# Performance work log

Measured on AMD Instinct MI355X. Metric: run time of the kernel, lower is better.

## Reference

```python
import jax, jax.numpy as jnp
import numpy as np

HEADS = 8
D_MODEL = 512
D_K = D_MODEL // HEADS


def setup_inputs() -> dict:
    key = jax.random.key(0)
    ks = jax.random.split(key, 12)
    B, S = 2, 4096
    scale = 1.0 / np.sqrt(D_MODEL)
    inp = {
        "q": jax.random.normal(ks[0], (B, S, D_MODEL), jnp.float32),
        "k": jax.random.normal(ks[1], (B, S, D_MODEL), jnp.float32),
        "v": jax.random.normal(ks[2], (B, S, D_MODEL), jnp.float32),
        "mask": jax.random.randint(ks[3], (B, 1, 1, S), 0, 2, jnp.int32),
        "wq": jax.random.normal(ks[4], (D_MODEL, D_MODEL), jnp.float32) * scale,
        "bq": jnp.zeros((D_MODEL,), jnp.float32),
        "wk": jax.random.normal(ks[5], (D_MODEL, D_MODEL), jnp.float32) * scale,
        "bk": jnp.zeros((D_MODEL,), jnp.float32),
        "wv": jax.random.normal(ks[6], (D_MODEL, D_MODEL), jnp.float32) * scale,
        "bv": jnp.zeros((D_MODEL,), jnp.float32),
        "wo": jax.random.normal(ks[7], (D_MODEL, D_MODEL), jnp.float32) * scale,
        "bo": jnp.zeros((D_MODEL,), jnp.float32),
    }
    return inp


def reference(q, k, v, mask, wq, bq, wk, bk, wv, bv, wo, bo):
    B, S, _ = q.shape
    # torch nn.Linear: y = x @ W.T + b
    qh = (q @ wq.T + bq).reshape(B, S, HEADS, D_K).transpose(0, 2, 1, 3)  # b h s d
    kh = (k @ wk.T + bk).reshape(B, S, HEADS, D_K).transpose(0, 2, 1, 3)
    vh = (v @ wv.T + bv).reshape(B, S, HEADS, D_K).transpose(0, 2, 1, 3)
    scores = jnp.einsum("bhqd,bhkd->bhqk", qh, kh) / jnp.sqrt(jnp.float32(D_K))
    scores = jnp.where(mask == 0, jnp.float32(-1e9), scores)
    attn = jax.nn.softmax(scores, axis=-1)  # dropout is identity in eval mode
    out = jnp.einsum("bhqk,bhkd->bhqd", attn, vh)
    out = out.transpose(0, 2, 1, 3).reshape(B, S, D_MODEL)
    return out @ wo.T + bo
```

## Files before the change

### kernel.cpp

```cpp
#include <hip/hip_runtime.h>
#include <hip/hip_bf16.h>

#define S 4096
#define DM 512
#define HH 8
#define DK 64
#define MT 8192

typedef __attribute__((ext_vector_type(8)))  short bf16x8;
typedef __attribute__((ext_vector_type(4)))  float f32x4;
typedef __attribute__((ext_vector_type(16))) float f32x16;
typedef __attribute__((ext_vector_type(4)))  unsigned int u32x4;

#define CQ 0.18033688011112042f

__device__ __forceinline__ short f2bs(float x) {
    __hip_bfloat16 h = __float2bfloat16(x);
    return *reinterpret_cast<short*>(&h);
}

__device__ __forceinline__ bf16x8 pack8(const float4& a, const float4& b) {
    bf16x8 r;
    r[0] = f2bs(a.x); r[1] = f2bs(a.y); r[2] = f2bs(a.z); r[3] = f2bs(a.w);
    r[4] = f2bs(b.x); r[5] = f2bs(b.y); r[6] = f2bs(b.z); r[7] = f2bs(b.w);
    return r;
}

__device__ __forceinline__ unsigned cvtpk(float lo, float hi) {
    unsigned r;
    asm("v_cvt_pk_bf16_f32 %0, %1, %2" : "=v"(r) : "v"(lo), "v"(hi));
    return r;
}

__device__ __forceinline__ bf16x8 mk_pb(unsigned a, unsigned b, unsigned c, unsigned d) {
    u32x4 t; t[0] = a; t[1] = b; t[2] = c; t[3] = d;
    return __builtin_bit_cast(bf16x8, t);
}

__device__ __forceinline__ void gld_lds16(const void* gp, void* lp) {
    __builtin_amdgcn_global_load_lds(
        (const __attribute__((address_space(1))) void*)gp,
        (__attribute__((address_space(3))) void*)lp, 16, 0, 0);
}

__global__ __launch_bounds__(256, 4)
void qkv_gemm(const float* __restrict__ Xq, const float* __restrict__ Xk,
              const float* __restrict__ Xv,
              const float* __restrict__ Wq, const float* __restrict__ Wk,
              const float* __restrict__ Wv,
              const float* __restrict__ Bq, const float* __restrict__ Bk,
              const float* __restrict__ Bv,
              const int* __restrict__ mask, float* __restrict__ maskf,
              unsigned short* __restrict__ Yq, unsigned short* __restrict__ Yk,
              unsigned short* __restrict__ Yv)
{
    __shared__ char As[128 * 128];
    __shared__ char Bs[64 * 128];
    const int bid  = blockIdx.x;
    const int t = threadIdx.x;
    if (bid < 32) {
        int i = bid * 256 + t;
        maskf[i] = mask[i] ? 0.f : -3e38f;
    }
    const int work = (bid & 7) * 192 + (bid >> 3);
    const int gp   = work >> 3;
    const int mat  = gp >> 6;
    const int m0   = (gp & 63) * 128;
    const int n0   = (work & 7) * 64;
    const float* X    = mat == 0 ? Xq : (mat == 1 ? Xk : Xv);
    const float* W    = mat == 0 ? Wq : (mat == 1 ? Wk : Wv);
    const float* bias = mat == 0 ? Bq : (mat == 1 ? Bk : Bv);

    const int l = t & 63, w = t >> 6;
    const int wr = w >> 1, wc = w & 1;
    const int lr = l & 15, lg = l >> 4;
    const int srow = t >> 3, schk = t & 7;
    const int sswz = (schk ^ (srow & 7)) * 16;

    float4 fA[4][2]; float4 fB[2][2];
    auto loadA = [&](int k0) {
        #pragma unroll
        for (int i = 0; i < 4; ++i) {
            const float* p = X + (size_t)(m0 + srow + 32 * i) * DM + k0 + schk * 8;
            fA[i][0] = *(const float4*)p;
            fA[i][1] = *(const float4*)(p + 4);
        }
    };
    auto loadB = [&](int k0) {
        #pragma unroll
        for (int i = 0; i < 2; ++i) {
            const float* p = W + (size_t)(n0 + srow + 32 * i) * DM + k0 + schk * 8;
            fB[i][0] = *(const float4*)p;
            fB[i][1] = *(const float4*)(p + 4);
        }
    };

    loadA(0); loadB(0);

    f32x4 acc[4][2];
    #pragma unroll
    for (int fm = 0; fm < 4; ++fm)
        #pragma unroll
        for (int fn = 0; fn < 2; ++fn) acc[fm][fn] = f32x4{0.f, 0.f, 0.f, 0.f};

    #pragma unroll
    for (int kt = 0; kt < 8; ++kt) {
        bf16x8 wA[4], wB[2];
        #pragma unroll
        for (int i = 0; i < 4; ++i) wA[i] = pack8(fA[i][0], fA[i][1]);
        #pragma unroll
        for (int i = 0; i < 2; ++i) wB[i] = pack8(fB[i][0], fB[i][1]);

        if (kt < 7) { loadA((kt + 1) * 64); loadB((kt + 1) * 64); }

        __syncthreads();
        #pragma unroll
        for (int i = 0; i < 4; ++i)
            *(bf16x8*)(As + (srow + 32 * i) * 128 + sswz) = wA[i];
        #pragma unroll
        for (int i = 0; i < 2; ++i)
            *(bf16x8*)(Bs + (srow + 32 * i) * 128 + sswz) = wB[i];
        __syncthreads();

        #pragma unroll
        for (int kc = 0; kc < 2; ++kc) {
            bf16x8 af[4], bfr[2];
            #pragma unroll
            for (int fm = 0; fm < 4; ++fm) {
                int row = wr * 64 + fm * 16 + lr;
                af[fm] = *(const bf16x8*)(As + row * 128 + (((kc * 4 + lg) ^ (row & 7)) * 16));
            }
            #pragma unroll
            for (int fn = 0; fn < 2; ++fn) {
                int row = wc * 32 + fn * 16 + lr;
                bfr[fn] = *(const bf16x8*)(Bs + row * 128 + (((kc * 4 + lg) ^ (row & 7)) * 16));
            }
            #pragma unroll
            for (int fm = 0; fm < 4; ++fm)
                #pragma unroll
                for (int fn = 0; fn < 2; ++fn)
                    acc[fm][fn] = __builtin_amdgcn_mfma_f32_16x16x32_bf16(af[fm], bfr[fn], acc[fm][fn], 0, 0, 0);
        }
    }

    #pragma unroll
    for (int fm = 0; fm < 4; ++fm) {
        #pragma unroll
        for (int fn = 0; fn < 2; ++fn) {
            int n = n0 + wc * 32 + fn * 16 + lr;
            float bn = bias[n];
            int mbase = m0 + wr * 64 + fm * 16 + lg * 4;
            int h = n >> 6, d = n & 63;
            int bb = mbase >> 12, s0 = mbase & (S - 1);
            if (mat == 0) {
                #pragma unroll
                for (int r = 0; r < 4; ++r)
                    Yq[(((size_t)(bb * HH + h)) * S + s0 + r) * DK + d] =
                        (unsigned short)f2bs((acc[fm][fn][r] + bn) * CQ);
            } else if (mat == 1) {
                int c   = (d >> 4) & 3;
                int hi2 = (d >> 3) & 1;
                int ii  = d & 7;
                size_t blkb = ((((size_t)(bb * HH + h)) * 128 + (s0 >> 5)) * 4 + c) * 512;
                int lanebase = (s0 & 31) + 32 * hi2;
                #pragma unroll
                for (int r = 0; r < 4; ++r)
                    Yk[blkb + (size_t)(lanebase + r) * 8 + ii] =
                        (unsigned short)f2bs(acc[fm][fn][r] + bn);
            } else {
                int dt2  = (d >> 5) & 1;
                int hi_s = (s0 >> 3) & 1;
                int lane = (d & 31) + 32 * hi_s;
                size_t base = ((((size_t)(bb * HH + h)) * 256 + (s0 >> 4)) * 2 + dt2) * 512
                            + (size_t)lane * 8 + (s0 & 7);
                ushort4 u;
                u.x = (unsigned short)f2bs(acc[fm][fn][0] + bn);
                u.y = (unsigned short)f2bs(acc[fm][fn][1] + bn);
                u.z = (unsigned short)f2bs(acc[fm][fn][2] + bn);
                u.w = (unsigned short)f2bs(acc[fm][fn][3] + bn);
                *(ushort4*)(Yv + base) = u;
            }
        }
    }
}

__global__ __launch_bounds__(256, 2)
void out_gemm(const short* __restrict__ Xb, const float* __restrict__ W,
              const float* __restrict__ bias, float* __restrict__ Y)
{
    __shared__ char As[128 * 128];
    __shared__ char Bs[64 * 128];
    const int bid  = blockIdx.x;
    const int work = (bid & 7) * 64 + (bid >> 3);
    const int n0 = (work & 7) * 64;
    const int m0 = (work >> 3) * 128;

    const int t = threadIdx.x, l = t & 63, w = t >> 6;
    const int wr = w >> 1, wc = w & 1;
    const int lr = l & 15, lg = l >> 4;
    const int srow = t >> 3, schk = t & 7;
    const int sswz = (schk ^ (srow & 7)) * 16;

    float4 fB[2][2]; bf16x8 rA[4];
    auto loadA = [&](int k0) {
        #pragma unroll
        for (int i = 0; i < 4; ++i)
            rA[i] = *(const bf16x8*)(Xb + (size_t)(m0 + srow + 32 * i) * DM + k0 + schk * 8);
    };
    auto loadB = [&](int k0) {
        #pragma unroll
        for (int i = 0; i < 2; ++i) {
            const float* p = W + (size_t)(n0 + srow + 32 * i) * DM + k0 + schk * 8;
            fB[i][0] = *(const float4*)p;
            fB[i][1] = *(const float4*)(p + 4);
        }
    };

    loadA(0); loadB(0);

    f32x4 acc[4][2];
    #pragma unroll
    for (int fm = 0; fm < 4; ++fm)
        #pragma unroll
        for (int fn = 0; fn < 2; ++fn) acc[fm][fn] = f32x4{0.f, 0.f, 0.f, 0.f};

    #pragma unroll
    for (int kt = 0; kt < 8; ++kt) {
        bf16x8 wA[4], wB[2];
        #pragma unroll
        for (int i = 0; i < 4; ++i) wA[i] = rA[i];
        #pragma unroll
        for (int i = 0; i < 2; ++i) wB[i] = pack8(fB[i][0], fB[i][1]);

        if (kt < 7) { loadA((kt + 1) * 64); loadB((kt + 1) * 64); }

        __syncthreads();
        #pragma unroll
        for (int i = 0; i < 4; ++i)
            *(bf16x8*)(As + (srow + 32 * i) * 128 + sswz) = wA[i];
        #pragma unroll
        for (int i = 0; i < 2; ++i)
            *(bf16x8*)(Bs + (srow + 32 * i) * 128 + sswz) = wB[i];
        __syncthreads();

        #pragma unroll
        for (int kc = 0; kc < 2; ++kc) {
            bf16x8 af[4], bfr[2];
            #pragma unroll
            for (int fm = 0; fm < 4; ++fm) {
                int row = wr * 64 + fm * 16 + lr;
                af[fm] = *(const bf16x8*)(As + row * 128 + (((kc * 4 + lg) ^ (row & 7)) * 16));
            }
            #pragma unroll
            for (int fn = 0; fn < 2; ++fn) {
                int row = wc * 32 + fn * 16 + lr;
                bfr[fn] = *(const bf16x8*)(Bs + row * 128 + (((kc * 4 + lg) ^ (row & 7)) * 16));
            }
            #pragma unroll
            for (int fm = 0; fm < 4; ++fm)
                #pragma unroll
                for (int fn = 0; fn < 2; ++fn)
                    acc[fm][fn] = __builtin_amdgcn_mfma_f32_16x16x32_bf16(af[fm], bfr[fn], acc[fm][fn], 0, 0, 0);
        }
    }

    #pragma unroll
    for (int fm = 0; fm < 4; ++fm) {
        #pragma unroll
        for (int fn = 0; fn < 2; ++fn) {
            int n = n0 + wc * 32 + fn * 16 + lr;
            float bn = bias[n];
            int mbase = m0 + wr * 64 + fm * 16 + lg * 4;
            #pragma unroll
            for (int r = 0; r < 4; ++r)
                Y[(size_t)(mbase + r) * DM + n] = acc[fm][fn][r] + bn;
        }
    }
}

__global__ __launch_bounds__(512, 4)
void flash_mfma(const short* __restrict__ qh,
                const short* __restrict__ kfb,
                const short* __restrict__ vfb,
                const float* __restrict__ maskf,
                unsigned short* __restrict__ att)
{
    const int bid  = blockIdx.x;
    const int work = (bid & 7) * 64 + (bid >> 3);
    const int bh = work >> 5, b = bh >> 3, h = bh & 7;
    const int q0 = (work & 31) * 128;
    const int t = threadIdx.x, w = t >> 6, l = t & 63;
    const int l31 = l & 31, hi = l >> 5;
    const int kw = w & 1, qw = w >> 1;

    __shared__ char sBuf[34048];
    char* B0 = sBuf;
    char* B1 = sBuf + 16384;

    const short* qg = qh + ((size_t)bh * S + q0 + qw * 32 + l31) * DK;
    bf16x8 qf[4];
    #pragma unroll
    for (int c = 0; c < 4; ++c)
        qf[c] = *(const bf16x8*)(qg + c * 16 + hi * 8);

    f32x16 oc[2];
    #pragma unroll
    for (int dt = 0; dt < 2; ++dt)
        #pragma unroll
        for (int r = 0; r < 16; ++r) oc[dt][r] = 0.f;
    float ls = 0.f;

    const char* kg0 = (const char*)(kfb + (size_t)bh * 262144) + (size_t)l * 16;
    const char* vg0 = (const char*)(vfb + (size_t)bh * 262144) + (size_t)l * 16;
    const float* mbase_g = maskf + b * S + kw * 32 + hi * 4;

    auto stage = [&](char* dst, int step) {
        const char* kg = kg0 + (size_t)step * 8192;
        const char* vg = vg0 + (size_t)step * 8192;
        #pragma unroll
        for (int i = 0; i < 2; ++i) {
            int chunk = w * 2 + i;
            const char* g = (chunk < 8) ? (kg + chunk * 1024) : (vg + (chunk - 8) * 1024);
            gld_lds16(g, dst + chunk * 1024);
        }
    };

    auto compute = [&](const char* kv, int step) {
        const float* mp = mbase_g + step * 64;
        f32x16 sc;
        float* scp = (float*)&sc;
        *(f32x4*)(scp + 0)  = *(const f32x4*)(mp);
        *(f32x4*)(scp + 4)  = *(const f32x4*)(mp + 8);
        *(f32x4*)(scp + 8)  = *(const f32x4*)(mp + 16);
        *(f32x4*)(scp + 12) = *(const f32x4*)(mp + 24);

        const char* kbase = kv + kw * 4096 + l * 16;
        bf16x8 kf0 = *(const bf16x8*)(kbase);
        bf16x8 kf1 = *(const bf16x8*)(kbase + 1024);
        bf16x8 kf2 = *(const bf16x8*)(kbase + 2048);
        bf16x8 kf3 = *(const bf16x8*)(kbase + 3072);
        __builtin_amdgcn_s_setprio(1);
        sc = __builtin_amdgcn_mfma_f32_32x32x16_bf16(kf0, qf[0], sc, 0, 0, 0);
        sc = __builtin_amdgcn_mfma_f32_32x32x16_bf16(kf1, qf[1], sc, 0, 0, 0);
        sc = __builtin_amdgcn_mfma_f32_32x32x16_bf16(kf2, qf[2], sc, 0, 0, 0);
        sc = __builtin_amdgcn_mfma_f32_32x32x16_bf16(kf3, qf[3], sc, 0, 0, 0);
        __builtin_amdgcn_s_setprio(0);

        const char* vbase = kv + 8192 + kw * 4096 + l * 16;
        bf16x8 vf00 = *(const bf16x8*)(vbase);
        bf16x8 vf01 = *(const bf16x8*)(vbase + 1024);
        bf16x8 vf10 = *(const bf16x8*)(vbase + 2048);
        bf16x8 vf11 = *(const bf16x8*)(vbase + 3072);

        float p[16];
        #pragma unroll
        for (int r = 0; r < 16; ++r) p[r] = exp2f(sc[r]);
        float a0 = 0.f;
        #pragma unroll
        for (int r = 0; r < 16; r += 4)
            a0 += (p[r] + p[r + 1]) + (p[r + 2] + p[r + 3]);
        ls += a0;

        unsigned A0 = cvtpk(p[0],  p[1]),  B0r = cvtpk(p[2],  p[3]);
        unsigned A1 = cvtpk(p[4],  p[5]),  B1r = cvtpk(p[6],  p[7]);
        unsigned A2 = cvtpk(p[8],  p[9]),  B2r = cvtpk(p[10], p[11]);
        unsigned A3 = cvtpk(p[12], p[13]), B3r = cvtpk(p[14], p[15]);
        asm("v_permlane32_swap_b32 %0, %1" : "+v"(A0), "+v"(A1));
        asm("v_permlane32_swap_b32 %0, %1" : "+v"(B0r), "+v"(B1r));
        asm("v_permlane32_swap_b32 %0, %1" : "+v"(A2), "+v"(A3));
        asm("v_permlane32_swap_b32 %0, %1" : "+v"(B2r), "+v"(B3r));
        bf16x8 pb0 = mk_pb(A0, B0r, A1, B1r);
        bf16x8 pb1 = mk_pb(A2, B2r, A3, B3r);

        __builtin_amdgcn_s_setprio(1);
        oc[0] = __builtin_amdgcn_mfma_f32_32x32x16_bf16(vf00, pb0, oc[0], 0, 0, 0);
        oc[1] = __builtin_amdgcn_mfma_f32_32x32x16_bf16(vf01, pb0, oc[1], 0, 0, 0);
        oc[0] = __builtin_amdgcn_mfma_f32_32x32x16_bf16(vf10, pb1, oc[0], 0, 0, 0);
        oc[1] = __builtin_amdgcn_mfma_f32_32x32x16_bf16(vf11, pb1, oc[1], 0, 0, 0);
        __builtin_amdgcn_s_setprio(0);
    };

    stage(B0, 0);
    __syncthreads();

    const int NT = S / 64;
    for (int it = 0; it < NT / 2; ++it) {
        const int s0 = it * 2;
        stage(B1, s0 + 1);
        compute(B0, s0);
        __syncthreads();
        if (s0 + 2 < NT) stage(B0, s0 + 2);
        compute(B1, s0 + 1);
        __syncthreads();
    }

    float* scr = (float*)sBuf;
    float* pp  = scr + (size_t)(qw * 64 + l) * 33;
    if (kw == 1) {
        #pragma unroll
        for (int r = 0; r < 16; ++r) { pp[r] = oc[0][r]; pp[16 + r] = oc[1][r]; }
        pp[32] = ls;
    }
    __syncthreads();
    if (kw == 0) {
        #pragma unroll
        for (int r = 0; r < 16; ++r) { oc[0][r] += pp[r]; oc[1][r] += pp[16 + r]; }
        ls += pp[32];
        ls += __shfl_xor(ls, 32);
        const float linv = 1.0f / ls;
        unsigned short* ap = att + ((size_t)(b * S + q0 + qw * 32 + l31)) * DM + h * DK;
        #pragma unroll
        for (int dt = 0; dt < 2; ++dt)
            #pragma unroll
            for (int g = 0; g < 4; ++g) {
                uint2 u;
                u.x = cvtpk(oc[dt][g * 4 + 0] * linv, oc[dt][g * 4 + 1] * linv);
                u.y = cvtpk(oc[dt][g * 4 + 2] * linv, oc[dt][g * 4 + 3] * linv);
                *(uint2*)(ap + dt * 32 + g * 8 + hi * 4) = u;
            }
    }
}

extern "C" void kernel_launch(void* const* d_in, const int* in_sizes, int n_in,
                              void* d_out, int out_size, void* d_ws, size_t ws_size,
                              hipStream_t stream) {
    const float* q    = (const float*)d_in[0];
    const float* k    = (const float*)d_in[1];
    const float* v    = (const float*)d_in[2];
    const int*   mask = (const int*)  d_in[3];
    const float* wq   = (const float*)d_in[4];
    const float* bq   = (const float*)d_in[5];
    const float* wk   = (const float*)d_in[6];
    const float* bk   = (const float*)d_in[7];
    const float* wv   = (const float*)d_in[8];
    const float* bv   = (const float*)d_in[9];
    const float* wo   = (const float*)d_in[10];
    const float* bo   = (const float*)d_in[11];
    float* out = (float*)d_out;

    char* wsb = (char*)d_ws;
    unsigned short* qh    = (unsigned short*)(wsb);
    unsigned short* kfb   = (unsigned short*)(wsb + (size_t)8  * 1024 * 1024);
    unsigned short* vfb   = (unsigned short*)(wsb + (size_t)16 * 1024 * 1024);
    unsigned short* att   = (unsigned short*)(wsb + (size_t)24 * 1024 * 1024);
    float*          maskf = (float*)         (wsb + (size_t)32 * 1024 * 1024);

    dim3 blk(256);
    qkv_gemm<<<dim3(1536), blk, 0, stream>>>(q, k, v, wq, wk, wv, bq, bk, bv,
                                     mask, maskf, qh, kfb, vfb);

    flash_mfma<<<dim3(512), dim3(512), 0, stream>>>((const short*)qh, (const short*)kfb,
                                     (const short*)vfb, maskf, att);

    out_gemm<<<dim3(512), blk, 0, stream>>>((const short*)att, wo, bo, out);
}
```

Before: 163.6 us.

## Software-pipeline QK and softmax-PV across tiles; halve flash block to 256 threads

The flash attention kernel now runs 256-thread blocks covering 64 queries each, with twice as many blocks, and each warp stages four chunks per tile. The loop is restructured so the QK^T MFMAs for the next KV tile are issued before the softmax and PV MFMAs of the current tile, keeping two score accumulators and two V fragment sets live. This is meant to overlap exp/convert work with matrix ops and improve scheduling across the GPU. In exchange it raises register pressure, drops the occupancy hint in launch bounds, and doubles K/V reads from global memory per query.

```diff
diff --git a/kernel.cpp b/kernel.cpp
--- a/kernel.cpp
+++ b/kernel.cpp
@@ -278,7 +278,7 @@
     }
 }
 
-__global__ __launch_bounds__(512, 4)
+__global__ __launch_bounds__(256)
 void flash_mfma(const short* __restrict__ qh,
                 const short* __restrict__ kfb,
                 const short* __restrict__ vfb,
@@ -286,14 +286,14 @@
                 unsigned short* __restrict__ att)
 {
     const int bid  = blockIdx.x;
-    const int work = (bid & 7) * 64 + (bid >> 3);
-    const int bh = work >> 5, b = bh >> 3, h = bh & 7;
-    const int q0 = (work & 31) * 128;
+    const int work = (bid & 7) * 128 + (bid >> 3);
+    const int bh = work >> 6, b = bh >> 3, h = bh & 7;
+    const int q0 = (work & 63) * 64;
     const int t = threadIdx.x, w = t >> 6, l = t & 63;
     const int l31 = l & 31, hi = l >> 5;
     const int kw = w & 1, qw = w >> 1;
 
-    __shared__ char sBuf[34048];
+    __shared__ char sBuf[33792];
     char* B0 = sBuf;
     char* B1 = sBuf + 16384;
 
@@ -318,14 +318,27 @@
         const char* kg = kg0 + (size_t)step * 8192;
         const char* vg = vg0 + (size_t)step * 8192;
         #pragma unroll
-        for (int i = 0; i < 2; ++i) {
-            int chunk = w * 2 + i;
+        for (int i = 0; i < 4; ++i) {
+            int chunk = w * 4 + i;
             const char* g = (chunk < 8) ? (kg + chunk * 1024) : (vg + (chunk - 8) * 1024);
             gld_lds16(g, dst + chunk * 1024);
         }
     };
 
-    auto compute = [&](const char* kv, int step) {
+    auto loadfrags = [&](const char* kv, bf16x8* kf, bf16x8* vf) {
+        const char* kbase = kv + kw * 4096 + l * 16;
+        kf[0] = *(const bf16x8*)(kbase);
+        kf[1] = *(const bf16x8*)(kbase + 1024);
+        kf[2] = *(const bf16x8*)(kbase + 2048);
+        kf[3] = *(const bf16x8*)(kbase + 3072);
+        const char* vbase = kv + 8192 + kw * 4096 + l * 16;
+        vf[0] = *(const bf16x8*)(vbase);
+        vf[1] = *(const bf16x8*)(vbase + 1024);
+        vf[2] = *(const bf16x8*)(vbase + 2048);
+        vf[3] = *(const bf16x8*)(vbase + 3072);
+    };
+
+    auto qk = [&](const bf16x8* kf, int step) -> f32x16 {
         const float* mp = mbase_g + step * 64;
         f32x16 sc;
         float* scp = (float*)&sc;
@@ -333,25 +346,16 @@
         *(f32x4*)(scp + 4)  = *(const f32x4*)(mp + 8);
         *(f32x4*)(scp + 8)  = *(const f32x4*)(mp + 16);
         *(f32x4*)(scp + 12) = *(const f32x4*)(mp + 24);
-
-        const char* kbase = kv + kw * 4096 + l * 16;
-        bf16x8 kf0 = *(const bf16x8*)(kbase);
-        bf16x8 kf1 = *(const bf16x8*)(kbase + 1024);
-        bf16x8 kf2 = *(const bf16x8*)(kbase + 2048);
-        bf16x8 kf3 = *(const bf16x8*)(kbase + 3072);
         __builtin_amdgcn_s_setprio(1);
-        sc = __builtin_amdgcn_mfma_f32_32x32x16_bf16(kf0, qf[0], sc, 0, 0, 0);
-        sc = __builtin_amdgcn_mfma_f32_32x32x16_bf16(kf1, qf[1], sc, 0, 0, 0);
-        sc = __builtin_amdgcn_mfma_f32_32x32x16_bf16(kf2, qf[2], sc, 0, 0, 0);
-        sc = __builtin_amdgcn_mfma_f32_32x32x16_bf16(kf3, qf[3], sc, 0, 0, 0);
+        sc = __builtin_amdgcn_mfma_f32_32x32x16_bf16(kf[0], qf[0], sc, 0, 0, 0);
+        sc = __builtin_amdgcn_mfma_f32_32x32x16_bf16(kf[1], qf[1], sc, 0, 0, 0);
+        sc = __builtin_amdgcn_mfma_f32_32x32x16_bf16(kf[2], qf[2], sc, 0, 0, 0);
+        sc = __builtin_amdgcn_mfma_f32_32x32x16_bf16(kf[3], qf[3], sc, 0, 0, 0);
         __builtin_amdgcn_s_setprio(0);
-
-        const char* vbase = kv + 8192 + kw * 4096 + l * 16;
-        bf16x8 vf00 = *(const bf16x8*)(vbase);
-        bf16x8 vf01 = *(const bf16x8*)(vbase + 1024);
-        bf16x8 vf10 = *(const bf16x8*)(vbase + 2048);
-        bf16x8 vf11 = *(const bf16x8*)(vbase + 3072);
-
+        return sc;
+    };
+
+    auto sm_pv = [&](const f32x16& sc, const bf16x8* vf) {
         float p[16];
         #pragma unroll
         for (int r = 0; r < 16; ++r) p[r] = exp2f(sc[r]);
@@ -373,27 +377,49 @@
         bf16x8 pb1 = mk_pb(A2, B2r, A3, B3r);
 
         __builtin_amdgcn_s_setprio(1);
-        oc[0] = __builtin_amdgcn_mfma_f32_32x32x16_bf16(vf00, pb0, oc[0], 0, 0, 0);
-        oc[1] = __builtin_amdgcn_mfma_f32_32x32x16_bf16(vf01, pb0, oc[1], 0, 0, 0);
-        oc[0] = __builtin_amdgcn_mfma_f32_32x32x16_bf16(vf10, pb1, oc[0], 0, 0, 0);
-        oc[1] = __builtin_amdgcn_mfma_f32_32x32x16_bf16(vf11, pb1, oc[1], 0, 0, 0);
+        oc[0] = __builtin_amdgcn_mfma_f32_32x32x16_bf16(vf[0], pb0, oc[0], 0, 0, 0);
+        oc[1] = __builtin_amdgcn_mfma_f32_32x32x16_bf16(vf[1], pb0, oc[1], 0, 0, 0);
+        oc[0] = __builtin_amdgcn_mfma_f32_32x32x16_bf16(vf[2], pb1, oc[0], 0, 0, 0);
+        oc[1] = __builtin_amdgcn_mfma_f32_32x32x16_bf16(vf[3], pb1, oc[1], 0, 0, 0);
         __builtin_amdgcn_s_setprio(0);
     };
 
+    bf16x8 vfA[4], vfB[4];
+    f32x16 scA;
     stage(B0, 0);
     __syncthreads();
+    {
+        bf16x8 kf[4];
+        loadfrags(B0, kf, vfA);
+        scA = qk(kf, 0);
+    }
+    stage(B1, 1);
 
     const int NT = S / 64;
-    for (int it = 0; it < NT / 2; ++it) {
-        const int s0 = it * 2;
-        stage(B1, s0 + 1);
-        compute(B0, s0);
-        __syncthreads();
-        if (s0 + 2 < NT) stage(B0, s0 + 2);
-        compute(B1, s0 + 1);
-        __syncthreads();
-    }
-
+    for (int it2 = 0; it2 < NT / 2; ++it2) {
+        const int it = it2 * 2;
+
+        __syncthreads();
+        f32x16 scB;
+        {
+            bf16x8 kf[4];
+            loadfrags(B1, kf, vfB);
+            scB = qk(kf, it + 1);
+        }
+        if (it + 2 < NT) stage(B0, it + 2);
+        sm_pv(scA, vfA);
+
+        __syncthreads();
+        if (it + 2 < NT) {
+            bf16x8 kf[4];
+            loadfrags(B0, kf, vfA);
+            scA = qk(kf, it + 2);
+        }
+        if (it + 3 < NT) stage(B1, it + 3);
+        sm_pv(scB, vfB);
+    }
+
+    __syncthreads();
     float* scr = (float*)sBuf;
     float* pp  = scr + (size_t)(qw * 64 + l) * 33;
     if (kw == 1) {
@@ -449,7 +475,7 @@
     qkv_gemm<<<dim3(1536), blk, 0, stream>>>(q, k, v, wq, wk, wv, bq, bk, bv,
                                      mask, maskf, qh, kfb, vfb);
 
-    flash_mfma<<<dim3(512), dim3(512), 0, stream>>>((const short*)qh, (const short*)kfb,
+    flash_mfma<<<dim3(1024), blk, 0, stream>>>((const short*)qh, (const short*)kfb,
                                      (const short*)vfb, maskf, att);
 
     out_gemm<<<dim3(512), blk, 0, stream>>>((const short*)att, wo, bo, out);
```

After: 181.9 us. 11.1% more time.

## Drop KV-split across waves in flash kernel, each wave handles full 64-key tile

Applied to the files above, without the earlier changes.

The flash-attention kernel drops from 512 threads to 256 per block, so each wave now processes all 64 keys of a tile instead of splitting them between two waves. This removes the cross-wave LDS reduction and the extra barrier in the epilogue, and doubles the MFMA work per wave per tile. In exchange it halves the waves per block, lowering latency hiding and raising register pressure from the two score accumulators.

```diff
diff --git a/kernel.cpp b/kernel.cpp
--- a/kernel.cpp
+++ b/kernel.cpp
@@ -278,7 +278,7 @@
     }
 }
 
-__global__ __launch_bounds__(512, 4)
+__global__ __launch_bounds__(256, 4)
 void flash_mfma(const short* __restrict__ qh,
                 const short* __restrict__ kfb,
                 const short* __restrict__ vfb,
@@ -291,9 +291,9 @@
     const int q0 = (work & 31) * 128;
     const int t = threadIdx.x, w = t >> 6, l = t & 63;
     const int l31 = l & 31, hi = l >> 5;
-    const int kw = w & 1, qw = w >> 1;
-
-    __shared__ char sBuf[34048];
+    const int qw = w;
+
+    __shared__ char sBuf[32768];
     char* B0 = sBuf;
     char* B1 = sBuf + 16384;
 
@@ -312,14 +312,14 @@
 
     const char* kg0 = (const char*)(kfb + (size_t)bh * 262144) + (size_t)l * 16;
     const char* vg0 = (const char*)(vfb + (size_t)bh * 262144) + (size_t)l * 16;
-    const float* mbase_g = maskf + b * S + kw * 32 + hi * 4;
+    const float* mbase_g = maskf + b * S + hi * 4;
 
     auto stage = [&](char* dst, int step) {
         const char* kg = kg0 + (size_t)step * 8192;
         const char* vg = vg0 + (size_t)step * 8192;
         #pragma unroll
-        for (int i = 0; i < 2; ++i) {
-            int chunk = w * 2 + i;
+        for (int i = 0; i < 4; ++i) {
+            int chunk = w * 4 + i;
             const char* g = (chunk < 8) ? (kg + chunk * 1024) : (vg + (chunk - 8) * 1024);
             gld_lds16(g, dst + chunk * 1024);
         }
@@ -327,56 +327,101 @@
 
     auto compute = [&](const char* kv, int step) {
         const float* mp = mbase_g + step * 64;
-        f32x16 sc;
-        float* scp = (float*)&sc;
-        *(f32x4*)(scp + 0)  = *(const f32x4*)(mp);
-        *(f32x4*)(scp + 4)  = *(const f32x4*)(mp + 8);
-        *(f32x4*)(scp + 8)  = *(const f32x4*)(mp + 16);
-        *(f32x4*)(scp + 12) = *(const f32x4*)(mp + 24);
-
-        const char* kbase = kv + kw * 4096 + l * 16;
+        f32x16 sc0, sc1;
+        {
+            float* s0p = (float*)&sc0;
+            float* s1p = (float*)&sc1;
+            *(f32x4*)(s0p + 0)  = *(const f32x4*)(mp);
+            *(f32x4*)(s0p + 4)  = *(const f32x4*)(mp + 8);
+            *(f32x4*)(s0p + 8)  = *(const f32x4*)(mp + 16);
+            *(f32x4*)(s0p + 12) = *(const f32x4*)(mp + 24);
+            *(f32x4*)(s1p + 0)  = *(const f32x4*)(mp + 32);
+            *(f32x4*)(s1p + 4)  = *(const f32x4*)(mp + 40);
+            *(f32x4*)(s1p + 8)  = *(const f32x4*)(mp + 48);
+            *(f32x4*)(s1p + 12) = *(const f32x4*)(mp + 56);
+        }
+
+        const char* kbase = kv + l * 16;
         bf16x8 kf0 = *(const bf16x8*)(kbase);
+        bf16x8 kf4 = *(const bf16x8*)(kbase + 4096);
         bf16x8 kf1 = *(const bf16x8*)(kbase + 1024);
+        bf16x8 kf5 = *(const bf16x8*)(kbase + 5120);
         bf16x8 kf2 = *(const bf16x8*)(kbase + 2048);
+        bf16x8 kf6 = *(const bf16x8*)(kbase + 6144);
         bf16x8 kf3 = *(const bf16x8*)(kbase + 3072);
+        bf16x8 kf7 = *(const bf16x8*)(kbase + 7168);
         __builtin_amdgcn_s_setprio(1);
-        sc = __builtin_amdgcn_mfma_f32_32x32x16_bf16(kf0, qf[0], sc, 0, 0, 0);
-        sc = __builtin_amdgcn_mfma_f32_32x32x16_bf16(kf1, qf[1], sc, 0, 0, 0);
-        sc = __builtin_amdgcn_mfma_f32_32x32x16_bf16(kf2, qf[2], sc, 0, 0, 0);
-        sc = __builtin_amdgcn_mfma_f32_32x32x16_bf16(kf3, qf[3], sc, 0, 0, 0);
+        sc0 = __builtin_amdgcn_mfma_f32_32x32x16_bf16(kf0, qf[0], sc0, 0, 0, 0);
+        sc1 = __builtin_amdgcn_mfma_f32_32x32x16_bf16(kf4, qf[0], sc1, 0, 0, 0);
+        sc0 = __builtin_amdgcn_mfma_f32_32x32x16_bf16(kf1, qf[1], sc0, 0, 0, 0);
+        sc1 = __builtin_amdgcn_mfma_f32_32x32x16_bf16(kf5, qf[1], sc1, 0, 0, 0);
+        sc0 = __builtin_amdgcn_mfma_f32_32x32x16_bf16(kf2, qf[2], sc0, 0, 0, 0);
+        sc1 = __builtin_amdgcn_mfma_f32_32x32x16_bf16(kf6, qf[2], sc1, 0, 0, 0);
+        sc0 = __builtin_amdgcn_mfma_f32_32x32x16_bf16(kf3, qf[3], sc0, 0, 0, 0);
+        sc1 = __builtin_amdgcn_mfma_f32_32x32x16_bf16(kf7, qf[3], sc1, 0, 0, 0);
         __builtin_amdgcn_s_setprio(0);
 
-        const char* vbase = kv + 8192 + kw * 4096 + l * 16;
+        bf16x8 pbA0, pbA1, pbB0, pbB1;
+        {
+            float p[16];
+            #pragma unroll
+            for (int r = 0; r < 16; ++r) p[r] = exp2f(sc0[r]);
+            float a0 = 0.f;
+            #pragma unroll
+            for (int r = 0; r < 16; r += 4)
+                a0 += (p[r] + p[r + 1]) + (p[r + 2] + p[r + 3]);
+            ls += a0;
+            unsigned A0 = cvtpk(p[0],  p[1]),  B0r = cvtpk(p[2],  p[3]);
+            unsigned A1 = cvtpk(p[4],  p[5]),  B1r = cvtpk(p[6],  p[7]);
+            unsigned A2 = cvtpk(p[8],  p[9]),  B2r = cvtpk(p[10], p[11]);
+            unsigned A3 = cvtpk(p[12], p[13]), B3r = cvtpk(p[14], p[15]);
+            asm("v_permlane32_swap_b32 %0, %1" : "+v"(A0), "+v"(A1));
+            asm("v_permlane32_swap_b32 %0, %1" : "+v"(B0r), "+v"(B1r));
+            asm("v_permlane32_swap_b32 %0, %1" : "+v"(A2), "+v"(A3));
+            asm("v_permlane32_swap_b32 %0, %1" : "+v"(B2r), "+v"(B3r));
+            pbA0 = mk_pb(A0, B0r, A1, B1r);
+            pbA1 = mk_pb(A2, B2r, A3, B3r);
+        }
+        {
+            float p[16];
+            #pragma unroll
+            for (int r = 0; r < 16; ++r) p[r] = exp2f(sc1[r]);
+            float a0 = 0.f;
+            #pragma unroll
+            for (int r = 0; r < 16; r += 4)
+                a0 += (p[r] + p[r + 1]) + (p[r + 2] + p[r + 3]);
+            ls += a0;
+            unsigned A0 = cvtpk(p[0],  p[1]),  B0r = cvtpk(p[2],  p[3]);
+            unsigned A1 = cvtpk(p[4],  p[5]),  B1r = cvtpk(p[6],  p[7]);
+            unsigned A2 = cvtpk(p[8],  p[9]),  B2r = cvtpk(p[10], p[11]);
+            unsigned A3 = cvtpk(p[12], p[13]), B3r = cvtpk(p[14], p[15]);
+            asm("v_permlane32_swap_b32 %0, %1" : "+v"(A0), "+v"(A1));
+            asm("v_permlane32_swap_b32 %0, %1" : "+v"(B0r), "+v"(B1r));
+            asm("v_permlane32_swap_b32 %0, %1" : "+v"(A2), "+v"(A3));
+            asm("v_permlane32_swap_b32 %0, %1" : "+v"(B2r), "+v"(B3r));
+            pbB0 = mk_pb(A0, B0r, A1, B1r);
+            pbB1 = mk_pb(A2, B2r, A3, B3r);
+        }
+
+        const char* vbase = kv + 8192 + l * 16;
         bf16x8 vf00 = *(const bf16x8*)(vbase);
         bf16x8 vf01 = *(const bf16x8*)(vbase + 1024);
         bf16x8 vf10 = *(const bf16x8*)(vbase + 2048);
         bf16x8 vf11 = *(const bf16x8*)(vbase + 3072);
-
-        float p[16];
-        #pragma unroll
-        for (int r = 0; r < 16; ++r) p[r] = exp2f(sc[r]);
-        float a0 = 0.f;
-        #pragma unroll
-        for (int r = 0; r < 16; r += 4)
-            a0 += (p[r] + p[r + 1]) + (p[r + 2] + p[r + 3]);
-        ls += a0;
-
-        unsigned A0 = cvtpk(p[0],  p[1]),  B0r = cvtpk(p[2],  p[3]);
-        unsigned A1 = cvtpk(p[4],  p[5]),  B1r = cvtpk(p[6],  p[7]);
-        unsigned A2 = cvtpk(p[8],  p[9]),  B2r = cvtpk(p[10], p[11]);
-        unsigned A3 = cvtpk(p[12], p[13]), B3r = cvtpk(p[14], p[15]);
-        asm("v_permlane32_swap_b32 %0, %1" : "+v"(A0), "+v"(A1));
-        asm("v_permlane32_swap_b32 %0, %1" : "+v"(B0r), "+v"(B1r));
-        asm("v_permlane32_swap_b32 %0, %1" : "+v"(A2), "+v"(A3));
-        asm("v_permlane32_swap_b32 %0, %1" : "+v"(B2r), "+v"(B3r));
-        bf16x8 pb0 = mk_pb(A0, B0r, A1, B1r);
-        bf16x8 pb1 = mk_pb(A2, B2r, A3, B3r);
+        bf16x8 vf20 = *(const bf16x8*)(vbase + 4096);
+        bf16x8 vf21 = *(const bf16x8*)(vbase + 5120);
+        bf16x8 vf30 = *(const bf16x8*)(vbase + 6144);
+        bf16x8 vf31 = *(const bf16x8*)(vbase + 7168);
 
         __builtin_amdgcn_s_setprio(1);
-        oc[0] = __builtin_amdgcn_mfma_f32_32x32x16_bf16(vf00, pb0, oc[0], 0, 0, 0);
-        oc[1] = __builtin_amdgcn_mfma_f32_32x32x16_bf16(vf01, pb0, oc[1], 0, 0, 0);
-        oc[0] = __builtin_amdgcn_mfma_f32_32x32x16_bf16(vf10, pb1, oc[0], 0, 0, 0);
-        oc[1] = __builtin_amdgcn_mfma_f32_32x32x16_bf16(vf11, pb1, oc[1], 0, 0, 0);
+        oc[0] = __builtin_amdgcn_mfma_f32_32x32x16_bf16(vf00, pbA0, oc[0], 0, 0, 0);
+        oc[1] = __builtin_amdgcn_mfma_f32_32x32x16_bf16(vf01, pbA0, oc[1], 0, 0, 0);
+        oc[0] = __builtin_amdgcn_mfma_f32_32x32x16_bf16(vf10, pbA1, oc[0], 0, 0, 0);
+        oc[1] = __builtin_amdgcn_mfma_f32_32x32x16_bf16(vf11, pbA1, oc[1], 0, 0, 0);
+        oc[0] = __builtin_amdgcn_mfma_f32_32x32x16_bf16(vf20, pbB0, oc[0], 0, 0, 0);
+        oc[1] = __builtin_amdgcn_mfma_f32_32x32x16_bf16(vf21, pbB0, oc[1], 0, 0, 0);
+        oc[0] = __builtin_amdgcn_mfma_f32_32x32x16_bf16(vf30, pbB1, oc[0], 0, 0, 0);
+        oc[1] = __builtin_amdgcn_mfma_f32_32x32x16_bf16(vf31, pbB1, oc[1], 0, 0, 0);
         __builtin_amdgcn_s_setprio(0);
     };
 
@@ -394,31 +439,18 @@
         __syncthreads();
     }
 
-    float* scr = (float*)sBuf;
-    float* pp  = scr + (size_t)(qw * 64 + l) * 33;
-    if (kw == 1) {
-        #pragma unroll
-        for (int r = 0; r < 16; ++r) { pp[r] = oc[0][r]; pp[16 + r] = oc[1][r]; }
-        pp[32] = ls;
-    }
-    __syncthreads();
-    if (kw == 0) {
-        #pragma unroll
-        for (int r = 0; r < 16; ++r) { oc[0][r] += pp[r]; oc[1][r] += pp[16 + r]; }
-        ls += pp[32];
-        ls += __shfl_xor(ls, 32);
-        const float linv = 1.0f / ls;
-        unsigned short* ap = att + ((size_t)(b * S + q0 + qw * 32 + l31)) * DM + h * DK;
-        #pragma unroll
-        for (int dt = 0; dt < 2; ++dt)
-            #pragma unroll
-            for (int g = 0; g < 4; ++g) {
-                uint2 u;
-                u.x = cvtpk(oc[dt][g * 4 + 0] * linv, oc[dt][g * 4 + 1] * linv);
-                u.y = cvtpk(oc[dt][g * 4 + 2] * linv, oc[dt][g * 4 + 3] * linv);
-                *(uint2*)(ap + dt * 32 + g * 8 + hi * 4) = u;
-            }
-    }
+    ls += __shfl_xor(ls, 32);
+    const float linv = 1.0f / ls;
+    unsigned short* ap = att + ((size_t)(b * S + q0 + qw * 32 + l31)) * DM + h * DK;
+    #pragma unroll
+    for (int dt = 0; dt < 2; ++dt)
+        #pragma unroll
+        for (int g = 0; g < 4; ++g) {
+            uint2 u;
+            u.x = cvtpk(oc[dt][g * 4 + 0] * linv, oc[dt][g * 4 + 1] * linv);
+            u.y = cvtpk(oc[dt][g * 4 + 2] * linv, oc[dt][g * 4 + 3] * linv);
+            *(uint2*)(ap + dt * 32 + g * 8 + hi * 4) = u;
+        }
 }
 
 extern "C" void kernel_launch(void* const* d_in, const int* in_sizes, int n_in,
@@ -449,7 +481,7 @@
     qkv_gemm<<<dim3(1536), blk, 0, stream>>>(q, k, v, wq, wk, wv, bq, bk, bv,
                                      mask, maskf, qh, kfb, vfb);
 
-    flash_mfma<<<dim3(512), dim3(512), 0, stream>>>((const short*)qh, (const short*)kfb,
+    flash_mfma<<<dim3(512), blk, 0, stream>>>((const short*)qh, (const short*)kfb,
                                      (const short*)vfb, maskf, att);
 
     out_gemm<<<dim3(512), blk, 0, stream>>>((const short*)att, wo, bo, out);
```

New measurement: 213.0 us. 1.3x slower.
